# Kernel tuning notes

Measured on AMD Instinct MI355X. Metric: run time of the kernel, lower is better.

Reference implementation:

```python
import jax, jax.numpy as jnp
import numpy as np

ALPHAS = (0.1, 0.3, 0.6)
WEIGHTS = (0.5, 0.3, 0.2)
HUBER_MARGIN = 1.0
B, S = 2048, 8192


def setup_inputs() -> dict:
    key = jax.random.key(0)
    k1, k2 = jax.random.split(key)
    pred = jax.random.normal(k1, (B, S), dtype=jnp.float32)
    target = jax.random.normal(k2, (B, S), dtype=jnp.float32)
    return {"pred": pred, "target": target}


def _ema(x, alpha):
    # x: [B, S]; ema[0] = x[0]; ema[i] = alpha*x[i] + (1-alpha)*ema[i-1]
    x0 = x[:, 0]
    def step(carry, xi):
        nc = alpha * xi + (1.0 - alpha) * carry
        return nc, nc
    _, ys = jax.lax.scan(step, x0, x[:, 1:].T)  # ys: [S-1, B]
    return jnp.concatenate([x0[:, None], ys.T], axis=1)  # [B, S]


def _huber_loss(pred_delta, target_delta):
    dir_agreement = pred_delta * target_delta
    step_err = jnp.abs(pred_delta - target_delta)
    quad = jnp.square(jnp.maximum(HUBER_MARGIN - dir_agreement, 0.0)) / (2.0 * HUBER_MARGIN)
    return jnp.where(dir_agreement < 0, step_err, quad).mean(axis=1)  # [B]


def reference(pred, target):
    loss = jnp.zeros((pred.shape[0],), dtype=pred.dtype)
    for alpha, weight in zip(ALPHAS, WEIGHTS):
        pe = _ema(pred, alpha)
        te = _ema(target, alpha)
        pd = pe[:, 1:] - pe[:, :-1]
        td = te[:, 1:] - te[:, :-1]
        loss = loss + weight * _huber_loss(pd, td)
    return loss.mean()  # reduction='mean'
```

## Files before the change

kernel.cpp:

```cpp
#include <hip/hip_runtime.h>

#define B_ROWS 2048
#define S_LEN  8192
#define PER_LANE 16
#define CHUNK (64 * PER_LANE)
#define CPR (S_LEN / CHUNK)
#define TPB 256
#define WPB 4
#define NCHUNK (B_ROWS * CPR)
#define NBLOCKS (NCHUNK / WPB)
#define HALO 256

constexpr double cpowi(double b, int e) { double r = 1.0; for (int i = 0; i < e; ++i) r *= b; return r; }
constexpr float tof(double x) { return (x < 1.2e-38 && x > -1.2e-38) ? 0.0f : (float)x; }

#define W0f 0.9f
#define W1f 0.7f
#define W2f 0.4f
#define SE0 0.2f
#define SE1 0.6f
#define SE2 1.2f
constexpr float NA0 = -(0.1f * 0.1f);
constexpr float NA1 = -(0.3f * 0.3f);
constexpr float NA2 = -(0.6f * 0.6f);

constexpr float D0_1 = tof(cpowi(0.9, 16)),  D0_2 = tof(cpowi(0.9, 32));
constexpr float D0_4 = tof(cpowi(0.9, 64)),  D0_8 = tof(cpowi(0.9, 128));
constexpr float D1_1 = tof(cpowi(0.7, 16)),  D1_2 = tof(cpowi(0.7, 32));
constexpr float D2_1 = tof(cpowi(0.4, 16));
constexpr float H0_1 = tof(cpowi(0.9, 4)),   H0_2 = tof(cpowi(0.9, 8));
constexpr float H0_4 = tof(cpowi(0.9, 16)),  H0_8 = tof(cpowi(0.9, 32));
constexpr float H0_16 = tof(cpowi(0.9, 64)), H0_32 = tof(cpowi(0.9, 128));
constexpr float H1_1 = tof(cpowi(0.7, 4)),   H1_2 = tof(cpowi(0.7, 8));
constexpr float H1_4 = tof(cpowi(0.7, 16)),  H1_8 = tof(cpowi(0.7, 32));
constexpr float H1_16 = tof(cpowi(0.7, 64));
constexpr float H2_1 = tof(cpowi(0.4, 4)),   H2_2 = tof(cpowi(0.4, 8));
constexpr float H2_4 = tof(cpowi(0.4, 16));

#define L2_0 (-0.15200309344504997f)
#define L2_1 (-0.51457317282975830f)
#define L2_2 (-1.32192809488736230f)

__device__ __forceinline__ float scan6(float v, int lane, float d1, float d2, float d4,
                                       float d8, float d16, float d32) {
    float u;
    u = __shfl_up(v, 1);  v += (lane >= 1  ? d1  : 0.0f) * u;
    u = __shfl_up(v, 2);  v += (lane >= 2  ? d2  : 0.0f) * u;
    u = __shfl_up(v, 4);  v += (lane >= 4  ? d4  : 0.0f) * u;
    u = __shfl_up(v, 8);  v += (lane >= 8  ? d8  : 0.0f) * u;
    u = __shfl_up(v, 16); v += (lane >= 16 ? d16 : 0.0f) * u;
    u = __shfl_up(v, 32); v += (lane >= 32 ? d32 : 0.0f) * u;
    return v;
}
__device__ __forceinline__ float scan5(float v, int lane, float d1, float d2, float d4,
                                       float d8, float d16) {
    float u;
    u = __shfl_up(v, 1);  v += (lane >= 1  ? d1  : 0.0f) * u;
    u = __shfl_up(v, 2);  v += (lane >= 2  ? d2  : 0.0f) * u;
    u = __shfl_up(v, 4);  v += (lane >= 4  ? d4  : 0.0f) * u;
    u = __shfl_up(v, 8);  v += (lane >= 8  ? d8  : 0.0f) * u;
    u = __shfl_up(v, 16); v += (lane >= 16 ? d16 : 0.0f) * u;
    return v;
}
__device__ __forceinline__ float scan4(float v, int lane, float d1, float d2, float d4, float d8) {
    float u;
    u = __shfl_up(v, 1); v += (lane >= 1 ? d1 : 0.0f) * u;
    u = __shfl_up(v, 2); v += (lane >= 2 ? d2 : 0.0f) * u;
    u = __shfl_up(v, 4); v += (lane >= 4 ? d4 : 0.0f) * u;
    u = __shfl_up(v, 8); v += (lane >= 8 ? d8 : 0.0f) * u;
    return v;
}
__device__ __forceinline__ float scan3(float v, int lane, float d1, float d2, float d4) {
    float u;
    u = __shfl_up(v, 1); v += (lane >= 1 ? d1 : 0.0f) * u;
    u = __shfl_up(v, 2); v += (lane >= 2 ? d2 : 0.0f) * u;
    u = __shfl_up(v, 4); v += (lane >= 4 ? d4 : 0.0f) * u;
    return v;
}
__device__ __forceinline__ float scan2(float v, int lane, float d1, float d2) {
    float u;
    u = __shfl_up(v, 1); v += (lane >= 1 ? d1 : 0.0f) * u;
    u = __shfl_up(v, 2); v += (lane >= 2 ? d2 : 0.0f) * u;
    return v;
}
__device__ __forceinline__ float scan1(float v, int lane, float d1) {
    float u;
    u = __shfl_up(v, 1); v += (lane >= 1 ? d1 : 0.0f) * u;
    return v;
}

__global__ void __launch_bounds__(TPB, 5) msl_main(const float* __restrict__ pred,
                                                   const float* __restrict__ targ,
                                                   float* __restrict__ partial) {
    const int lane = threadIdx.x & 63;
    const int wave = threadIdx.x >> 6;
    const int gcid = blockIdx.x * WPB + wave;
    const int row  = gcid >> 3;
    const int cid  = gcid & (CPR - 1);
    const float* __restrict__ prow = pred + (size_t)row * S_LEN;
    const float* __restrict__ trow = targ + (size_t)row * S_LEN;
    const int co   = cid * CHUNK;
    const int base = co + lane * PER_LANE;

    __shared__ float dxs[WPB][2][PER_LANE - 1][64];
    __shared__ float sred[WPB];

    const bool lz     = (lane == 0);
    const bool haloed = (cid != 0);
    const bool head   = (!haloed) && lz;

    float xp[PER_LANE], xt[PER_LANE];
    {
        const float4* p4 = reinterpret_cast<const float4*>(prow + base);
        const float4* t4 = reinterpret_cast<const float4*>(trow + base);
#pragma unroll
        for (int j = 0; j < PER_LANE / 4; ++j) {
            float4 a = p4[j];
            float4 b = t4[j];
            xp[4 * j + 0] = a.x; xp[4 * j + 1] = a.y; xp[4 * j + 2] = a.z; xp[4 * j + 3] = a.w;
            xt[4 * j + 0] = b.x; xt[4 * j + 1] = b.y; xt[4 * j + 2] = b.z; xt[4 * j + 3] = b.w;
        }
    }

    float Cp0 = 0.f, Cp1 = 0.f, Cp2 = 0.f, Ct0 = 0.f, Ct1 = 0.f, Ct2 = 0.f;
    float lastp = xp[0], lastt = xt[0];
    if (haloed) {
        float hp[4], ht[4];
        {
            float4 a = *reinterpret_cast<const float4*>(prow + co - HALO + lane * 4);
            float4 b = *reinterpret_cast<const float4*>(trow + co - HALO + lane * 4);
            hp[0] = a.x; hp[1] = a.y; hp[2] = a.z; hp[3] = a.w;
            ht[0] = b.x; ht[1] = b.y; ht[2] = b.z; ht[3] = b.w;
        }
        float php = __shfl_up(hp[3], 1);
        float pht = __shfl_up(ht[3], 1);
        if (lz) { php = hp[0]; pht = ht[0]; }

        float Ap0 = 0.f, Ap1 = 0.f, Ap2 = 0.f, At0 = 0.f, At1 = 0.f, At2 = 0.f;
#pragma unroll
        for (int s = 0; s < 4; ++s) {
            float dxp = hp[s] - php; php = hp[s];
            float dxt = ht[s] - pht; pht = ht[s];
            Ap0 = fmaf(W0f, Ap0, dxp);
            Ap1 = fmaf(W1f, Ap1, dxp);
            Ap2 = fmaf(W2f, Ap2, dxp);
            At0 = fmaf(W0f, At0, dxt);
            At1 = fmaf(W1f, At1, dxt);
            At2 = fmaf(W2f, At2, dxt);
        }
        float vh;
        vh = scan6(Ap0, lane, H0_1, H0_2, H0_4, H0_8, H0_16, H0_32); Cp0 = __shfl(vh, 63);
        vh = scan5(Ap1, lane, H1_1, H1_2, H1_4, H1_8, H1_16);        Cp1 = __shfl(vh, 63);
        vh = scan3(Ap2, lane, H2_1, H2_2, H2_4);                     Cp2 = __shfl(vh, 63);
        vh = scan6(At0, lane, H0_1, H0_2, H0_4, H0_8, H0_16, H0_32); Ct0 = __shfl(vh, 63);
        vh = scan5(At1, lane, H1_1, H1_2, H1_4, H1_8, H1_16);        Ct1 = __shfl(vh, 63);
        vh = scan3(At2, lane, H2_1, H2_2, H2_4);                     Ct2 = __shfl(vh, 63);
        lastp = __shfl(hp[3], 63);
        lastt = __shfl(ht[3], 63);
    }

    float pvp = __shfl_up(xp[PER_LANE - 1], 1);
    float pvt = __shfl_up(xt[PER_LANE - 1], 1);
    if (lz) { pvp = lastp; pvt = lastt; }

    float dx0p, dx0t;
    float Mp0 = 0.f, Mp1 = 0.f, Mp2 = 0.f, Mt0 = 0.f, Mt1 = 0.f, Mt2 = 0.f;
#pragma unroll
    for (int j = 0; j < PER_LANE; ++j) {
        float dxp = xp[j] - pvp; pvp = xp[j];
        float dxt = xt[j] - pvt; pvt = xt[j];
        if (j == 0) { dx0p = dxp; dx0t = dxt; }
        else        { dxs[wave][0][j - 1][lane] = dxp; dxs[wave][1][j - 1][lane] = dxt; }
        Mp0 = fmaf(W0f, Mp0, dxp);
        Mp1 = fmaf(W1f, Mp1, dxp);
        Mp2 = fmaf(W2f, Mp2, dxp);
        Mt0 = fmaf(W0f, Mt0, dxt);
        Mt1 = fmaf(W1f, Mt1, dxt);
        Mt2 = fmaf(W2f, Mt2, dxt);
    }

    float vp0 = scan4(Mp0, lane, D0_1, D0_2, D0_4, D0_8);
    float vp1 = scan2(Mp1, lane, D1_1, D1_2);
    float vp2 = scan1(Mp2, lane, D2_1);
    float vt0 = scan4(Mt0, lane, D0_1, D0_2, D0_4, D0_8);
    float vt1 = scan2(Mt1, lane, D1_1, D1_2);
    float vt2 = scan1(Mt2, lane, D2_1);

    const float e  = (float)(PER_LANE * lane);
    const float G0 = exp2f(e * L2_0);
    const float G1 = exp2f(e * L2_1);
    const float G2 = exp2f(e * L2_2);

    float up0 = __shfl_up(vp0, 1), up1 = __shfl_up(vp1, 1), up2 = __shfl_up(vp2, 1);
    float ut0 = __shfl_up(vt0, 1), ut1 = __shfl_up(vt1, 1), ut2 = __shfl_up(vt2, 1);

    float yp0 = lz ? Cp0 : fmaf(G0, Cp0, up0);
    float yp1 = lz ? Cp1 : fmaf(G1, Cp1, up1);
    float yp2 = lz ? Cp2 : fmaf(G2, Cp2, up2);
    float yt0 = lz ? Ct0 : fmaf(G0, Ct0, ut0);
    float yt1 = lz ? Ct1 : fmaf(G1, Ct1, ut1);
    float yt2 = lz ? Ct2 : fmaf(G2, Ct2, ut2);

    float acc0 = 0.f, acc1 = 0.f, acc2 = 0.f;
    const float skip = head ? 0.0f : 1.0f;
#pragma unroll
    for (int j = 0; j < PER_LANE; ++j) {
        float dxp = (j == 0) ? dx0p : dxs[wave][0][j - 1][lane];
        float dxt = (j == 0) ? dx0t : dxs[wave][1][j - 1][lane];
        yp0 = fmaf(W0f, yp0, dxp);
        yt0 = fmaf(W0f, yt0, dxt);
        yp1 = fmaf(W1f, yp1, dxp);
        yt1 = fmaf(W1f, yt1, dxt);
        yp2 = fmaf(W2f, yp2, dxp);
        yt2 = fmaf(W2f, yt2, dxt);

        float m0 = yp0 * yt0, m1 = yp1 * yt1, m2 = yp2 * yt2;
        float se0 = SE0 * fabsf(yp0 - yt0);
        float se1 = SE1 * fabsf(yp1 - yt1);
        float se2 = SE2 * fabsf(yp2 - yt2);
        float mm0 = fmaxf(fmaf(NA0, m0, 1.0f), 0.0f);
        float mm1 = fmaxf(fmaf(NA1, m1, 1.0f), 0.0f);
        float mm2 = fmaxf(fmaf(NA2, m2, 1.0f), 0.0f);
        float h0 = (m0 < 0.0f) ? se0 : mm0 * mm0;
        float h1 = (m1 < 0.0f) ? se1 : mm1 * mm1;
        float h2 = (m2 < 0.0f) ? se2 : mm2 * mm2;
        if (j == 0) { h0 *= skip; h1 *= skip; h2 *= skip; }
        acc0 += h0; acc1 += h1; acc2 += h2;
    }

    float wacc = 0.25f * acc0 + 0.15f * acc1 + 0.10f * acc2;
#pragma unroll
    for (int o = 32; o > 0; o >>= 1) wacc += __shfl_down(wacc, o);

    if (lz) sred[wave] = wacc;
    __syncthreads();
    if (threadIdx.x == 0)
        partial[blockIdx.x] = sred[0] + sred[1] + sred[2] + sred[3];
}

__global__ void __launch_bounds__(256) msl_reduce(const float* __restrict__ partial,
                                                  float* __restrict__ out) {
    const int tid = threadIdx.x;
    float v = 0.f;
#pragma unroll
    for (int k = 0; k < NBLOCKS / 256; ++k) v += partial[tid + 256 * k];
#pragma unroll
    for (int o = 32; o > 0; o >>= 1) v += __shfl_down(v, o);
    __shared__ float s[4];
    if ((tid & 63) == 0) s[tid >> 6] = v;
    __syncthreads();
    if (tid == 0)
        out[0] = (s[0] + s[1] + s[2] + s[3]) *
                 (float)(1.0 / ((double)(S_LEN - 1) * (double)B_ROWS));
}

extern "C" void kernel_launch(void* const* d_in, const int* in_sizes, int n_in,
                              void* d_out, int out_size, void* d_ws, size_t ws_size,
                              hipStream_t stream) {
    const float* pred = (const float*)d_in[0];
    const float* targ = (const float*)d_in[1];
    float* out = (float*)d_out;
    float* partial = (float*)d_ws;

    msl_main<<<NBLOCKS, TPB, 0, stream>>>(pred, targ, partial);
    msl_reduce<<<1, 256, 0, stream>>>(partial, out);
}
```

Measured before the change: 143.7 us.

## Process two chunks per wave, carrying EMA state instead of halo recomputation

Each block now handles one full row, with each wave processing two consecutive 1024-element chunks. The EMA state and last sample from the first chunk feed the second directly, so half of the halo loads and halo scans go away. The LDS staging of differences is dropped; differences are recomputed from registers, and the block-level shared reduction is replaced by per-wave partial writes. In exchange, per-wave serial work doubles, the block count drops to 2048, and the 5-waves occupancy hint is removed, which could reduce latency hiding.

```diff
diff --git a/kernel.cpp b/kernel.cpp
--- a/kernel.cpp
+++ b/kernel.cpp
@@ -4,11 +4,11 @@
 #define S_LEN  8192
 #define PER_LANE 16
 #define CHUNK (64 * PER_LANE)
-#define CPR (S_LEN / CHUNK)
+#define CPW 2
+#define WPB 4
 #define TPB 256
-#define WPB 4
-#define NCHUNK (B_ROWS * CPR)
-#define NBLOCKS (NCHUNK / WPB)
+#define NBLOCKS B_ROWS
+#define NPART (NBLOCKS * WPB)
 #define HALO 256
 
 constexpr double cpowi(double b, int e) { double r = 1.0; for (int i = 0; i < e; ++i) r *= b; return r; }
@@ -89,46 +89,29 @@
     return v;
 }
 
-__global__ void __launch_bounds__(TPB, 5) msl_main(const float* __restrict__ pred,
-                                                   const float* __restrict__ targ,
-                                                   float* __restrict__ partial) {
+__global__ void __launch_bounds__(TPB) msl_main(const float* __restrict__ pred,
+                                                const float* __restrict__ targ,
+                                                float* __restrict__ partial) {
     const int lane = threadIdx.x & 63;
     const int wave = threadIdx.x >> 6;
-    const int gcid = blockIdx.x * WPB + wave;
-    const int row  = gcid >> 3;
-    const int cid  = gcid & (CPR - 1);
-    const float* __restrict__ prow = pred + (size_t)row * S_LEN;
-    const float* __restrict__ trow = targ + (size_t)row * S_LEN;
-    const int co   = cid * CHUNK;
-    const int base = co + lane * PER_LANE;
-
-    __shared__ float dxs[WPB][2][PER_LANE - 1][64];
-    __shared__ float sred[WPB];
-
-    const bool lz     = (lane == 0);
-    const bool haloed = (cid != 0);
-    const bool head   = (!haloed) && lz;
-
-    float xp[PER_LANE], xt[PER_LANE];
-    {
-        const float4* p4 = reinterpret_cast<const float4*>(prow + base);
-        const float4* t4 = reinterpret_cast<const float4*>(trow + base);
-#pragma unroll
-        for (int j = 0; j < PER_LANE / 4; ++j) {
-            float4 a = p4[j];
-            float4 b = t4[j];
-            xp[4 * j + 0] = a.x; xp[4 * j + 1] = a.y; xp[4 * j + 2] = a.z; xp[4 * j + 3] = a.w;
-            xt[4 * j + 0] = b.x; xt[4 * j + 1] = b.y; xt[4 * j + 2] = b.z; xt[4 * j + 3] = b.w;
-        }
-    }
+    const float* __restrict__ prow = pred + (size_t)blockIdx.x * S_LEN;
+    const float* __restrict__ trow = targ + (size_t)blockIdx.x * S_LEN;
+    const bool lz = (lane == 0);
+    const bool w0 = (wave == 0);
+
+    const float e  = (float)(PER_LANE * lane);
+    const float G0 = exp2f(e * L2_0);
+    const float G1 = exp2f(e * L2_1);
+    const float G2 = exp2f(e * L2_2);
 
     float Cp0 = 0.f, Cp1 = 0.f, Cp2 = 0.f, Ct0 = 0.f, Ct1 = 0.f, Ct2 = 0.f;
-    float lastp = xp[0], lastt = xt[0];
-    if (haloed) {
+    float lastp = 0.f, lastt = 0.f;
+    if (wave > 0) {
+        const int co0 = wave * CPW * CHUNK;
         float hp[4], ht[4];
         {
-            float4 a = *reinterpret_cast<const float4*>(prow + co - HALO + lane * 4);
-            float4 b = *reinterpret_cast<const float4*>(trow + co - HALO + lane * 4);
+            float4 a = *reinterpret_cast<const float4*>(prow + co0 - HALO + lane * 4);
+            float4 b = *reinterpret_cast<const float4*>(trow + co0 - HALO + lane * 4);
             hp[0] = a.x; hp[1] = a.y; hp[2] = a.z; hp[3] = a.w;
             ht[0] = b.x; ht[1] = b.y; ht[2] = b.z; ht[3] = b.w;
         }
@@ -159,83 +142,101 @@
         lastt = __shfl(ht[3], 63);
     }
 
-    float pvp = __shfl_up(xp[PER_LANE - 1], 1);
-    float pvt = __shfl_up(xt[PER_LANE - 1], 1);
-    if (lz) { pvp = lastp; pvt = lastt; }
-
-    float dx0p, dx0t;
-    float Mp0 = 0.f, Mp1 = 0.f, Mp2 = 0.f, Mt0 = 0.f, Mt1 = 0.f, Mt2 = 0.f;
-#pragma unroll
-    for (int j = 0; j < PER_LANE; ++j) {
-        float dxp = xp[j] - pvp; pvp = xp[j];
-        float dxt = xt[j] - pvt; pvt = xt[j];
-        if (j == 0) { dx0p = dxp; dx0t = dxt; }
-        else        { dxs[wave][0][j - 1][lane] = dxp; dxs[wave][1][j - 1][lane] = dxt; }
-        Mp0 = fmaf(W0f, Mp0, dxp);
-        Mp1 = fmaf(W1f, Mp1, dxp);
-        Mp2 = fmaf(W2f, Mp2, dxp);
-        Mt0 = fmaf(W0f, Mt0, dxt);
-        Mt1 = fmaf(W1f, Mt1, dxt);
-        Mt2 = fmaf(W2f, Mt2, dxt);
+    float acc0 = 0.f, acc1 = 0.f, acc2 = 0.f;
+
+#pragma unroll
+    for (int c = 0; c < CPW; ++c) {
+        const int base = (wave * CPW + c) * CHUNK + lane * PER_LANE;
+        float xp[PER_LANE], xt[PER_LANE];
+        {
+            const float4* p4 = reinterpret_cast<const float4*>(prow + base);
+            const float4* t4 = reinterpret_cast<const float4*>(trow + base);
+#pragma unroll
+            for (int j = 0; j < PER_LANE / 4; ++j) {
+                float4 a = p4[j];
+                float4 b = t4[j];
+                xp[4 * j + 0] = a.x; xp[4 * j + 1] = a.y; xp[4 * j + 2] = a.z; xp[4 * j + 3] = a.w;
+                xt[4 * j + 0] = b.x; xt[4 * j + 1] = b.y; xt[4 * j + 2] = b.z; xt[4 * j + 3] = b.w;
+            }
+        }
+
+        float pvp = __shfl_up(xp[PER_LANE - 1], 1);
+        float pvt = __shfl_up(xt[PER_LANE - 1], 1);
+        if (lz) {
+            pvp = (w0 && c == 0) ? xp[0] : lastp;
+            pvt = (w0 && c == 0) ? xt[0] : lastt;
+        }
+
+        float Mp0 = 0.f, Mp1 = 0.f, Mp2 = 0.f, Mt0 = 0.f, Mt1 = 0.f, Mt2 = 0.f;
+        float pp = pvp, pt = pvt;
+#pragma unroll
+        for (int j = 0; j < PER_LANE; ++j) {
+            float dxp = xp[j] - pp; pp = xp[j];
+            float dxt = xt[j] - pt; pt = xt[j];
+            Mp0 = fmaf(W0f, Mp0, dxp);
+            Mp1 = fmaf(W1f, Mp1, dxp);
+            Mp2 = fmaf(W2f, Mp2, dxp);
+            Mt0 = fmaf(W0f, Mt0, dxt);
+            Mt1 = fmaf(W1f, Mt1, dxt);
+            Mt2 = fmaf(W2f, Mt2, dxt);
+        }
+
+        float vp0 = scan4(Mp0, lane, D0_1, D0_2, D0_4, D0_8);
+        float vp1 = scan2(Mp1, lane, D1_1, D1_2);
+        float vp2 = scan1(Mp2, lane, D2_1);
+        float vt0 = scan4(Mt0, lane, D0_1, D0_2, D0_4, D0_8);
+        float vt1 = scan2(Mt1, lane, D1_1, D1_2);
+        float vt2 = scan1(Mt2, lane, D2_1);
+
+        float up0 = __shfl_up(vp0, 1), up1 = __shfl_up(vp1, 1), up2 = __shfl_up(vp2, 1);
+        float ut0 = __shfl_up(vt0, 1), ut1 = __shfl_up(vt1, 1), ut2 = __shfl_up(vt2, 1);
+
+        float yp0 = lz ? Cp0 : fmaf(G0, Cp0, up0);
+        float yp1 = lz ? Cp1 : fmaf(G1, Cp1, up1);
+        float yp2 = lz ? Cp2 : fmaf(G2, Cp2, up2);
+        float yt0 = lz ? Ct0 : fmaf(G0, Ct0, ut0);
+        float yt1 = lz ? Ct1 : fmaf(G1, Ct1, ut1);
+        float yt2 = lz ? Ct2 : fmaf(G2, Ct2, ut2);
+
+        const float skip = (w0 && c == 0 && lz) ? 0.0f : 1.0f;
+        pp = pvp; pt = pvt;
+#pragma unroll
+        for (int j = 0; j < PER_LANE; ++j) {
+            float dxp = xp[j] - pp; pp = xp[j];
+            float dxt = xt[j] - pt; pt = xt[j];
+            yp0 = fmaf(W0f, yp0, dxp);
+            yt0 = fmaf(W0f, yt0, dxt);
+            yp1 = fmaf(W1f, yp1, dxp);
+            yt1 = fmaf(W1f, yt1, dxt);
+            yp2 = fmaf(W2f, yp2, dxp);
+            yt2 = fmaf(W2f, yt2, dxt);
+
+            float m0 = yp0 * yt0, m1 = yp1 * yt1, m2 = yp2 * yt2;
+            float se0 = SE0 * fabsf(yp0 - yt0);
+            float se1 = SE1 * fabsf(yp1 - yt1);
+            float se2 = SE2 * fabsf(yp2 - yt2);
+            float mm0 = fmaxf(fmaf(NA0, m0, 1.0f), 0.0f);
+            float mm1 = fmaxf(fmaf(NA1, m1, 1.0f), 0.0f);
+            float mm2 = fmaxf(fmaf(NA2, m2, 1.0f), 0.0f);
+            float h0 = (m0 < 0.0f) ? se0 : mm0 * mm0;
+            float h1 = (m1 < 0.0f) ? se1 : mm1 * mm1;
+            float h2 = (m2 < 0.0f) ? se2 : mm2 * mm2;
+            if (j == 0) { h0 *= skip; h1 *= skip; h2 *= skip; }
+            acc0 += h0; acc1 += h1; acc2 += h2;
+        }
+
+        if (c + 1 < CPW) {
+            Cp0 = __shfl(yp0, 63); Cp1 = __shfl(yp1, 63); Cp2 = __shfl(yp2, 63);
+            Ct0 = __shfl(yt0, 63); Ct1 = __shfl(yt1, 63); Ct2 = __shfl(yt2, 63);
+            lastp = __shfl(xp[PER_LANE - 1], 63);
+            lastt = __shfl(xt[PER_LANE - 1], 63);
+        }
     }
 
-    float vp0 = scan4(Mp0, lane, D0_1, D0_2, D0_4, D0_8);
-    float vp1 = scan2(Mp1, lane, D1_1, D1_2);
-    float vp2 = scan1(Mp2, lane, D2_1);
-    float vt0 = scan4(Mt0, lane, D0_1, D0_2, D0_4, D0_8);
-    float vt1 = scan2(Mt1, lane, D1_1, D1_2);
-    float vt2 = scan1(Mt2, lane, D2_1);
-
-    const float e  = (float)(PER_LANE * lane);
-    const float G0 = exp2f(e * L2_0);
-    const float G1 = exp2f(e * L2_1);
-    const float G2 = exp2f(e * L2_2);
-
-    float up0 = __shfl_up(vp0, 1), up1 = __shfl_up(vp1, 1), up2 = __shfl_up(vp2, 1);
-    float ut0 = __shfl_up(vt0, 1), ut1 = __shfl_up(vt1, 1), ut2 = __shfl_up(vt2, 1);
-
-    float yp0 = lz ? Cp0 : fmaf(G0, Cp0, up0);
-    float yp1 = lz ? Cp1 : fmaf(G1, Cp1, up1);
-    float yp2 = lz ? Cp2 : fmaf(G2, Cp2, up2);
-    float yt0 = lz ? Ct0 : fmaf(G0, Ct0, ut0);
-    float yt1 = lz ? Ct1 : fmaf(G1, Ct1, ut1);
-    float yt2 = lz ? Ct2 : fmaf(G2, Ct2, ut2);
-
-    float acc0 = 0.f, acc1 = 0.f, acc2 = 0.f;
-    const float skip = head ? 0.0f : 1.0f;
-#pragma unroll
-    for (int j = 0; j < PER_LANE; ++j) {
-        float dxp = (j == 0) ? dx0p : dxs[wave][0][j - 1][lane];
-        float dxt = (j == 0) ? dx0t : dxs[wave][1][j - 1][lane];
-        yp0 = fmaf(W0f, yp0, dxp);
-        yt0 = fmaf(W0f, yt0, dxt);
-        yp1 = fmaf(W1f, yp1, dxp);
-        yt1 = fmaf(W1f, yt1, dxt);
-        yp2 = fmaf(W2f, yp2, dxp);
-        yt2 = fmaf(W2f, yt2, dxt);
-
-        float m0 = yp0 * yt0, m1 = yp1 * yt1, m2 = yp2 * yt2;
-        float se0 = SE0 * fabsf(yp0 - yt0);
-        float se1 = SE1 * fabsf(yp1 - yt1);
-        float se2 = SE2 * fabsf(yp2 - yt2);
-        float mm0 = fmaxf(fmaf(NA0, m0, 1.0f), 0.0f);
-        float mm1 = fmaxf(fmaf(NA1, m1, 1.0f), 0.0f);
-        float mm2 = fmaxf(fmaf(NA2, m2, 1.0f), 0.0f);
-        float h0 = (m0 < 0.0f) ? se0 : mm0 * mm0;
-        float h1 = (m1 < 0.0f) ? se1 : mm1 * mm1;
-        float h2 = (m2 < 0.0f) ? se2 : mm2 * mm2;
-        if (j == 0) { h0 *= skip; h1 *= skip; h2 *= skip; }
-        acc0 += h0; acc1 += h1; acc2 += h2;
-    }
-
     float wacc = 0.25f * acc0 + 0.15f * acc1 + 0.10f * acc2;
 #pragma unroll
     for (int o = 32; o > 0; o >>= 1) wacc += __shfl_down(wacc, o);
-
-    if (lz) sred[wave] = wacc;
-    __syncthreads();
-    if (threadIdx.x == 0)
-        partial[blockIdx.x] = sred[0] + sred[1] + sred[2] + sred[3];
+    if (lz) partial[blockIdx.x * WPB + wave] = wacc;
 }
 
 __global__ void __launch_bounds__(256) msl_reduce(const float* __restrict__ partial,
@@ -243,7 +244,7 @@
     const int tid = threadIdx.x;
     float v = 0.f;
 #pragma unroll
-    for (int k = 0; k < NBLOCKS / 256; ++k) v += partial[tid + 256 * k];
+    for (int k = 0; k < NPART / 256; ++k) v += partial[tid + 256 * k];
 #pragma unroll
     for (int o = 32; o > 0; o >>= 1) v += __shfl_down(v, o);
     __shared__ float s[4];
```

New measurement: 148.3 us. +3.2%, slower.

## Use 64 elements per lane, half-row per wave, reload from global instead of LDS

Applied to the files above, without the earlier changes.

Each wave now covers half a row with 64 elements per lane, where before it covered a 1024-element chunk with 16 per lane. Longer per-lane spans shorten or remove the cross-lane scans, because decays for alpha 0.3 and 0.6 underflow over 64 steps. The LDS staging of deltas is dropped: the second pass re-reads the inputs from global memory and counts on cache hits. The block-level sync is also removed, with one partial written per wave. The cost is longer serial dependency chains per lane, fewer waves in flight (only 4096 in total), and the halo cost being paid only once per row.

```diff
diff --git a/kernel.cpp b/kernel.cpp
--- a/kernel.cpp
+++ b/kernel.cpp
@@ -2,13 +2,13 @@
 
 #define B_ROWS 2048
 #define S_LEN  8192
-#define PER_LANE 16
-#define CHUNK (64 * PER_LANE)
-#define CPR (S_LEN / CHUNK)
+#define PL 64
+#define WELEMS (64 * PL)
 #define TPB 256
 #define WPB 4
-#define NCHUNK (B_ROWS * CPR)
-#define NBLOCKS (NCHUNK / WPB)
+#define NWAVES (B_ROWS * 2)
+#define NBLOCKS (NWAVES / WPB)
+#define NST 4
 #define HALO 256
 
 constexpr double cpowi(double b, int e) { double r = 1.0; for (int i = 0; i < e; ++i) r *= b; return r; }
@@ -24,10 +24,7 @@
 constexpr float NA1 = -(0.3f * 0.3f);
 constexpr float NA2 = -(0.6f * 0.6f);
 
-constexpr float D0_1 = tof(cpowi(0.9, 16)),  D0_2 = tof(cpowi(0.9, 32));
-constexpr float D0_4 = tof(cpowi(0.9, 64)),  D0_8 = tof(cpowi(0.9, 128));
-constexpr float D1_1 = tof(cpowi(0.7, 16)),  D1_2 = tof(cpowi(0.7, 32));
-constexpr float D2_1 = tof(cpowi(0.4, 16));
+constexpr float E0_1 = tof(cpowi(0.9, 64)), E0_2 = tof(cpowi(0.9, 128));
 constexpr float H0_1 = tof(cpowi(0.9, 4)),   H0_2 = tof(cpowi(0.9, 8));
 constexpr float H0_4 = tof(cpowi(0.9, 16)),  H0_8 = tof(cpowi(0.9, 32));
 constexpr float H0_16 = tof(cpowi(0.9, 64)), H0_32 = tof(cpowi(0.9, 128));
@@ -38,8 +35,6 @@
 constexpr float H2_4 = tof(cpowi(0.4, 16));
 
 #define L2_0 (-0.15200309344504997f)
-#define L2_1 (-0.51457317282975830f)
-#define L2_2 (-1.32192809488736230f)
 
 __device__ __forceinline__ float scan6(float v, int lane, float d1, float d2, float d4,
                                        float d8, float d16, float d32) {
@@ -62,69 +57,36 @@
     u = __shfl_up(v, 16); v += (lane >= 16 ? d16 : 0.0f) * u;
     return v;
 }
-__device__ __forceinline__ float scan4(float v, int lane, float d1, float d2, float d4, float d8) {
+__device__ __forceinline__ float scan3(float v, int lane, float d1, float d2, float d4) {
     float u;
     u = __shfl_up(v, 1); v += (lane >= 1 ? d1 : 0.0f) * u;
     u = __shfl_up(v, 2); v += (lane >= 2 ? d2 : 0.0f) * u;
     u = __shfl_up(v, 4); v += (lane >= 4 ? d4 : 0.0f) * u;
-    u = __shfl_up(v, 8); v += (lane >= 8 ? d8 : 0.0f) * u;
-    return v;
-}
-__device__ __forceinline__ float scan3(float v, int lane, float d1, float d2, float d4) {
+    return v;
+}
+__device__ __forceinline__ float scan2(float v, int lane, float d1, float d2) {
     float u;
     u = __shfl_up(v, 1); v += (lane >= 1 ? d1 : 0.0f) * u;
     u = __shfl_up(v, 2); v += (lane >= 2 ? d2 : 0.0f) * u;
-    u = __shfl_up(v, 4); v += (lane >= 4 ? d4 : 0.0f) * u;
-    return v;
-}
-__device__ __forceinline__ float scan2(float v, int lane, float d1, float d2) {
-    float u;
-    u = __shfl_up(v, 1); v += (lane >= 1 ? d1 : 0.0f) * u;
-    u = __shfl_up(v, 2); v += (lane >= 2 ? d2 : 0.0f) * u;
-    return v;
-}
-__device__ __forceinline__ float scan1(float v, int lane, float d1) {
-    float u;
-    u = __shfl_up(v, 1); v += (lane >= 1 ? d1 : 0.0f) * u;
-    return v;
-}
-
-__global__ void __launch_bounds__(TPB, 5) msl_main(const float* __restrict__ pred,
+    return v;
+}
+
+__global__ void __launch_bounds__(TPB, 4) msl_main(const float* __restrict__ pred,
                                                    const float* __restrict__ targ,
                                                    float* __restrict__ partial) {
     const int lane = threadIdx.x & 63;
     const int wave = threadIdx.x >> 6;
-    const int gcid = blockIdx.x * WPB + wave;
-    const int row  = gcid >> 3;
-    const int cid  = gcid & (CPR - 1);
+    const int wid  = blockIdx.x * WPB + wave;
+    const int row  = wid >> 1;
+    const int half = wid & 1;
     const float* __restrict__ prow = pred + (size_t)row * S_LEN;
     const float* __restrict__ trow = targ + (size_t)row * S_LEN;
-    const int co   = cid * CHUNK;
-    const int base = co + lane * PER_LANE;
-
-    __shared__ float dxs[WPB][2][PER_LANE - 1][64];
-    __shared__ float sred[WPB];
-
-    const bool lz     = (lane == 0);
-    const bool haloed = (cid != 0);
-    const bool head   = (!haloed) && lz;
-
-    float xp[PER_LANE], xt[PER_LANE];
-    {
-        const float4* p4 = reinterpret_cast<const float4*>(prow + base);
-        const float4* t4 = reinterpret_cast<const float4*>(trow + base);
-#pragma unroll
-        for (int j = 0; j < PER_LANE / 4; ++j) {
-            float4 a = p4[j];
-            float4 b = t4[j];
-            xp[4 * j + 0] = a.x; xp[4 * j + 1] = a.y; xp[4 * j + 2] = a.z; xp[4 * j + 3] = a.w;
-            xt[4 * j + 0] = b.x; xt[4 * j + 1] = b.y; xt[4 * j + 2] = b.z; xt[4 * j + 3] = b.w;
-        }
-    }
+    const int co   = half * WELEMS;
+    const bool lz   = (lane == 0);
+    const bool head = (half == 0) && lz;
 
     float Cp0 = 0.f, Cp1 = 0.f, Cp2 = 0.f, Ct0 = 0.f, Ct1 = 0.f, Ct2 = 0.f;
-    float lastp = xp[0], lastt = xt[0];
-    if (haloed) {
+    if (half) {
         float hp[4], ht[4];
         {
             float4 a = *reinterpret_cast<const float4*>(prow + co - HALO + lane * 4);
@@ -155,87 +117,104 @@
         vh = scan6(At0, lane, H0_1, H0_2, H0_4, H0_8, H0_16, H0_32); Ct0 = __shfl(vh, 63);
         vh = scan5(At1, lane, H1_1, H1_2, H1_4, H1_8, H1_16);        Ct1 = __shfl(vh, 63);
         vh = scan3(At2, lane, H2_1, H2_2, H2_4);                     Ct2 = __shfl(vh, 63);
-        lastp = __shfl(hp[3], 63);
-        lastt = __shfl(ht[3], 63);
     }
 
-    float pvp = __shfl_up(xp[PER_LANE - 1], 1);
-    float pvt = __shfl_up(xt[PER_LANE - 1], 1);
-    if (lz) { pvp = lastp; pvt = lastt; }
-
-    float dx0p, dx0t;
+    const int poff = co + lane * PL - 1 + (head ? 1 : 0);
+    const float prevp = prow[poff];
+    const float prevt = trow[poff];
+
+    const float* pb = prow + co + lane * PL;
+    const float* tb = trow + co + lane * PL;
+
     float Mp0 = 0.f, Mp1 = 0.f, Mp2 = 0.f, Mt0 = 0.f, Mt1 = 0.f, Mt2 = 0.f;
-#pragma unroll
-    for (int j = 0; j < PER_LANE; ++j) {
-        float dxp = xp[j] - pvp; pvp = xp[j];
-        float dxt = xt[j] - pvt; pvt = xt[j];
-        if (j == 0) { dx0p = dxp; dx0t = dxt; }
-        else        { dxs[wave][0][j - 1][lane] = dxp; dxs[wave][1][j - 1][lane] = dxt; }
-        Mp0 = fmaf(W0f, Mp0, dxp);
-        Mp1 = fmaf(W1f, Mp1, dxp);
-        Mp2 = fmaf(W2f, Mp2, dxp);
-        Mt0 = fmaf(W0f, Mt0, dxt);
-        Mt1 = fmaf(W1f, Mt1, dxt);
-        Mt2 = fmaf(W2f, Mt2, dxt);
+    {
+        float pp = prevp, pt = prevt;
+#pragma unroll
+        for (int st = 0; st < NST; ++st) {
+            const float4* p4 = reinterpret_cast<const float4*>(pb + st * 16);
+            const float4* t4 = reinterpret_cast<const float4*>(tb + st * 16);
+#pragma unroll
+            for (int q = 0; q < 4; ++q) {
+                float4 a = p4[q];
+                float4 b = t4[q];
+#pragma unroll
+                for (int j = 0; j < 4; ++j) {
+                    float xpv = (&a.x)[j];
+                    float xtv = (&b.x)[j];
+                    float dxp = xpv - pp; pp = xpv;
+                    float dxt = xtv - pt; pt = xtv;
+                    Mp0 = fmaf(W0f, Mp0, dxp);
+                    Mp1 = fmaf(W1f, Mp1, dxp);
+                    Mp2 = fmaf(W2f, Mp2, dxp);
+                    Mt0 = fmaf(W0f, Mt0, dxt);
+                    Mt1 = fmaf(W1f, Mt1, dxt);
+                    Mt2 = fmaf(W2f, Mt2, dxt);
+                }
+            }
+        }
     }
 
-    float vp0 = scan4(Mp0, lane, D0_1, D0_2, D0_4, D0_8);
-    float vp1 = scan2(Mp1, lane, D1_1, D1_2);
-    float vp2 = scan1(Mp2, lane, D2_1);
-    float vt0 = scan4(Mt0, lane, D0_1, D0_2, D0_4, D0_8);
-    float vt1 = scan2(Mt1, lane, D1_1, D1_2);
-    float vt2 = scan1(Mt2, lane, D2_1);
-
-    const float e  = (float)(PER_LANE * lane);
-    const float G0 = exp2f(e * L2_0);
-    const float G1 = exp2f(e * L2_1);
-    const float G2 = exp2f(e * L2_2);
-
-    float up0 = __shfl_up(vp0, 1), up1 = __shfl_up(vp1, 1), up2 = __shfl_up(vp2, 1);
-    float ut0 = __shfl_up(vt0, 1), ut1 = __shfl_up(vt1, 1), ut2 = __shfl_up(vt2, 1);
+    float vp0 = scan2(Mp0, lane, E0_1, E0_2);
+    float vt0 = scan2(Mt0, lane, E0_1, E0_2);
+
+    const float G0 = exp2f((float)(PL * lane) * L2_0);
+    float up0 = __shfl_up(vp0, 1), ut0 = __shfl_up(vt0, 1);
+    float up1 = __shfl_up(Mp1, 1), ut1 = __shfl_up(Mt1, 1);
+    float up2 = __shfl_up(Mp2, 1), ut2 = __shfl_up(Mt2, 1);
 
     float yp0 = lz ? Cp0 : fmaf(G0, Cp0, up0);
-    float yp1 = lz ? Cp1 : fmaf(G1, Cp1, up1);
-    float yp2 = lz ? Cp2 : fmaf(G2, Cp2, up2);
     float yt0 = lz ? Ct0 : fmaf(G0, Ct0, ut0);
-    float yt1 = lz ? Ct1 : fmaf(G1, Ct1, ut1);
-    float yt2 = lz ? Ct2 : fmaf(G2, Ct2, ut2);
+    float yp1 = lz ? Cp1 : up1;
+    float yt1 = lz ? Ct1 : ut1;
+    float yp2 = lz ? Cp2 : up2;
+    float yt2 = lz ? Ct2 : ut2;
 
     float acc0 = 0.f, acc1 = 0.f, acc2 = 0.f;
     const float skip = head ? 0.0f : 1.0f;
-#pragma unroll
-    for (int j = 0; j < PER_LANE; ++j) {
-        float dxp = (j == 0) ? dx0p : dxs[wave][0][j - 1][lane];
-        float dxt = (j == 0) ? dx0t : dxs[wave][1][j - 1][lane];
-        yp0 = fmaf(W0f, yp0, dxp);
-        yt0 = fmaf(W0f, yt0, dxt);
-        yp1 = fmaf(W1f, yp1, dxp);
-        yt1 = fmaf(W1f, yt1, dxt);
-        yp2 = fmaf(W2f, yp2, dxp);
-        yt2 = fmaf(W2f, yt2, dxt);
-
-        float m0 = yp0 * yt0, m1 = yp1 * yt1, m2 = yp2 * yt2;
-        float se0 = SE0 * fabsf(yp0 - yt0);
-        float se1 = SE1 * fabsf(yp1 - yt1);
-        float se2 = SE2 * fabsf(yp2 - yt2);
-        float mm0 = fmaxf(fmaf(NA0, m0, 1.0f), 0.0f);
-        float mm1 = fmaxf(fmaf(NA1, m1, 1.0f), 0.0f);
-        float mm2 = fmaxf(fmaf(NA2, m2, 1.0f), 0.0f);
-        float h0 = (m0 < 0.0f) ? se0 : mm0 * mm0;
-        float h1 = (m1 < 0.0f) ? se1 : mm1 * mm1;
-        float h2 = (m2 < 0.0f) ? se2 : mm2 * mm2;
-        if (j == 0) { h0 *= skip; h1 *= skip; h2 *= skip; }
-        acc0 += h0; acc1 += h1; acc2 += h2;
+    {
+        float pp = prevp, pt = prevt;
+#pragma unroll
+        for (int st = 0; st < NST; ++st) {
+            const float4* p4 = reinterpret_cast<const float4*>(pb + st * 16);
+            const float4* t4 = reinterpret_cast<const float4*>(tb + st * 16);
+#pragma unroll
+            for (int q = 0; q < 4; ++q) {
+                float4 a = p4[q];
+                float4 b = t4[q];
+#pragma unroll
+                for (int j = 0; j < 4; ++j) {
+                    float xpv = (&a.x)[j];
+                    float xtv = (&b.x)[j];
+                    float dxp = xpv - pp; pp = xpv;
+                    float dxt = xtv - pt; pt = xtv;
+                    yp0 = fmaf(W0f, yp0, dxp);
+                    yt0 = fmaf(W0f, yt0, dxt);
+                    yp1 = fmaf(W1f, yp1, dxp);
+                    yt1 = fmaf(W1f, yt1, dxt);
+                    yp2 = fmaf(W2f, yp2, dxp);
+                    yt2 = fmaf(W2f, yt2, dxt);
+
+                    float m0 = yp0 * yt0, m1 = yp1 * yt1, m2 = yp2 * yt2;
+                    float se0 = SE0 * fabsf(yp0 - yt0);
+                    float se1 = SE1 * fabsf(yp1 - yt1);
+                    float se2 = SE2 * fabsf(yp2 - yt2);
+                    float mm0 = fmaxf(fmaf(NA0, m0, 1.0f), 0.0f);
+                    float mm1 = fmaxf(fmaf(NA1, m1, 1.0f), 0.0f);
+                    float mm2 = fmaxf(fmaf(NA2, m2, 1.0f), 0.0f);
+                    float h0 = (m0 < 0.0f) ? se0 : mm0 * mm0;
+                    float h1 = (m1 < 0.0f) ? se1 : mm1 * mm1;
+                    float h2 = (m2 < 0.0f) ? se2 : mm2 * mm2;
+                    if (st == 0 && q == 0 && j == 0) { h0 *= skip; h1 *= skip; h2 *= skip; }
+                    acc0 += h0; acc1 += h1; acc2 += h2;
+                }
+            }
+        }
     }
 
     float wacc = 0.25f * acc0 + 0.15f * acc1 + 0.10f * acc2;
 #pragma unroll
     for (int o = 32; o > 0; o >>= 1) wacc += __shfl_down(wacc, o);
-
-    if (lz) sred[wave] = wacc;
-    __syncthreads();
-    if (threadIdx.x == 0)
-        partial[blockIdx.x] = sred[0] + sred[1] + sred[2] + sred[3];
+    if (lz) partial[wid] = wacc;
 }
 
 __global__ void __launch_bounds__(256) msl_reduce(const float* __restrict__ partial,
@@ -243,7 +222,7 @@
     const int tid = threadIdx.x;
     float v = 0.f;
 #pragma unroll
-    for (int k = 0; k < NBLOCKS / 256; ++k) v += partial[tid + 256 * k];
+    for (int k = 0; k < NWAVES / 256; ++k) v += partial[tid + 256 * k];
 #pragma unroll
     for (int o = 32; o > 0; o >>= 1) v += __shfl_down(v, o);
     __shared__ float s[4];
```

Measured after the change: 258.6 us. 80.0% more time.
